# Performance work log

Measured on AMD Instinct MI355X. Metric: run time of the kernel, lower is better.

The kernel has to match this reference:

```python
import jax, jax.numpy as jnp
import numpy as np

B, F, NB, E = 32768, 64, 64, 32


def setup_inputs() -> dict:
    key = jax.random.key(0)
    k1, k2, k3, k4 = jax.random.split(key, 4)
    x = jax.random.normal(k1, (B, F), dtype=jnp.float32)
    # per-feature sorted bin edges (as produced by PLE.adapt quantiles)
    bins = jnp.sort(jax.random.uniform(k2, (F, NB), dtype=jnp.float32,
                                       minval=-2.0, maxval=2.0), axis=1)
    W = jax.random.normal(k3, (F, NB, E), dtype=jnp.float32) / np.sqrt(NB)
    b = jax.random.normal(k4, (F, E), dtype=jnp.float32)
    return {"x": x, "bins": bins, "W": W, "b": b}


def reference(x, bins, W, b):
    # x: [B,F], bins: [F,NB] sorted edges, W: [F,NB,E], b: [F,E]
    nb = bins.shape[1]
    lo = bins  # bins[j] == lookup_table[i-1] for bin i=j+1
    # lookup_table.get(i, -1): last bin has no upper edge -> defaults to -1.0
    hi = jnp.concatenate(
        [bins[:, 1:], jnp.full((bins.shape[0], 1), -1.0, bins.dtype)], axis=1)
    j = jnp.arange(nb)
    xe = x[:, :, None]                                  # [B,F,1]
    left = (xe < lo[None]) & (j > 0)                    # [B,F,NB]
    right = (xe >= hi[None]) & (j < nb - 1)             # [B,F,NB]
    v = (xe - lo[None]) / (hi - lo)[None]               # interpolation value
    # enc = 0 where left, 1 where neither, v where exactly one of left/right
    enc = jnp.where(left != right, v, jnp.where(left, 0.0, 1.0))  # [B,F,NB]
    # per-feature linear + ReLU, then features stacked along dim 1
    emb = jax.nn.relu(jnp.einsum('bfn,fne->bfe', enc, W) + b[None])  # [B,F,E]
    return emb
```

## Files before the change

kernel.cpp:

```cpp
#include <hip/hip_runtime.h>


#define FDIM 64
#define NB   64
#define EDIM 32
#define FSL  8
#define NRPB 256
#define WPAD 33
#define ITERS (NRPB / 32)

typedef __attribute__((ext_vector_type(4))) float f32x4;

__global__ __launch_bounds__(256) void nemb_fused(
    const float* __restrict__ x, const float* __restrict__ bins,
    const float* __restrict__ W, const float* __restrict__ bias,
    float* __restrict__ out)
{
    __shared__ float sW[FSL * NB * WPAD];
    __shared__ float sBins[FSL * 65];
    __shared__ float sg [FSL * NB];
    __shared__ float slg[FSL * NB];
    __shared__ float sP [FSL * EDIM];
    __shared__ float sR [FSL * EDIM];
    __shared__ float pX[4][64];
    __shared__ float pC[4][64];
    __shared__ int   pK[4][64];

    const int t     = threadIdx.x;
    const int slice = blockIdx.x & 7;
    const int chunk = blockIdx.x >> 3;
    const int f0    = slice * FSL;

    const int w  = t >> 6;
    const int l  = t & 63;
    const int rs = l >> 3;
    const int fs = l & 7;
    const int ft = l >> 3;
    const int e0 = (l & 7) * 4;

    const long r00 = (long)chunk * NRPB;

    float x_cur = x[(r00 + w * 8 + rs) * FDIM + f0 + fs];
    float bias_v = bias[(f0 + (t >> 5)) * EDIM + (t & 31)];

    {
        int idx = t * 2;
        int fl  = idx >> 6;
        int n   = idx & 63;
        const float* bg = bins + (size_t)(f0 + fl) * NB;
        float b0v = bg[n];
        float b1v = bg[n + 1];
        float b2v = (n + 1 == 63) ? -1.0f : bg[n + 2];
        float g0 = 1.0f / (b1v - b0v);
        float g1 = 1.0f / (b2v - b1v);
        sg [fl * NB + n]     = g0;
        sg [fl * NB + n + 1] = g1;
        slg[fl * NB + n]     = b0v * g0;
        slg[fl * NB + n + 1] = b1v * g1;
    }

    const float* Wg = W + (size_t)f0 * NB * EDIM;
    #pragma unroll
    for (int i = 0; i < 16; ++i) {
        int qi = i * 256 + t;
        f32x4 v = reinterpret_cast<const f32x4*>(Wg)[qi];
        int gi = qi * 4;
        int fl = gi >> 11;
        int n  = (gi >> 5) & 63;
        int ee = gi & 31;
        *reinterpret_cast<f32x4*>(&sW[fl * (NB * WPAD) + n * WPAD + ee]) = v;
    }
    if (t < 128) {
        f32x4 v = reinterpret_cast<const f32x4*>(bins + (size_t)f0 * NB)[t];
        int gi = t * 4;
        int fl = gi >> 6, n = gi & 63;
        float* d = &sBins[fl * 65 + n];
        d[0] = v.x; d[1] = v.y; d[2] = v.z; d[3] = v.w;
    }
    if (t < FSL) sBins[t * 65 + 64] = -1.0f;
    __syncthreads();

    {
        const int fl = t >> 5;
        const int e  = t & 31;
        const float* wrow = &sW[fl * (NB * WPAD) + e];
        const float* gr   = &sg [fl * NB];
        const float* lgr  = &slg[fl * NB];
        float p = 0.0f, q = 0.0f;
        #pragma unroll
        for (int n = 0; n < NB; ++n) {
            float wv = wrow[n * WPAD];
            p = fmaf(gr[n],  wv, p);
            q = fmaf(lgr[n], wv, q);
        }
        sP[fl * EDIM + e] = p;
        sR[fl * EDIM + e] = bias_v - q;
    }
    __syncthreads();

    const f32x4 Pv = *reinterpret_cast<const f32x4*>(&sP[ft * EDIM + e0]);
    const f32x4 Rv = *reinterpret_cast<const f32x4*>(&sR[ft * EDIM + e0]);

    const float* bl = &sBins[fs * 65];

    #pragma unroll 2
    for (int it = 0; it < ITERS; ++it) {
        const long rb = r00 + it * 32 + w * 8;

        float xv = x_cur;
        if (it + 1 < ITERS)
            x_cur = x[(rb + 32 + rs) * FDIM + f0 + fs];

        int k = 0;
        k += (bl[ 8] <= xv) ? 8 : 0;
        k += (bl[16] <= xv) ? 8 : 0;
        k += (bl[24] <= xv) ? 8 : 0;
        k += (bl[32] <= xv) ? 8 : 0;
        k += (bl[40] <= xv) ? 8 : 0;
        k += (bl[48] <= xv) ? 8 : 0;
        k += (bl[56] <= xv) ? 8 : 0;
        {
            const float* b2 = bl + k;
            int inner = 0;
            inner += (b2[1] <= xv) ? 1 : 0;
            inner += (b2[2] <= xv) ? 1 : 0;
            inner += (b2[3] <= xv) ? 1 : 0;
            inner += (b2[4] <= xv) ? 1 : 0;
            inner += (b2[5] <= xv) ? 1 : 0;
            inner += (b2[6] <= xv) ? 1 : 0;
            inner += (b2[7] <= xv) ? 1 : 0;
            k += inner;
        }
        float lo = bl[k];
        float hi = bl[k + 1];
        float cv = (hi - xv) * __builtin_amdgcn_rcpf(hi - lo);

        pX[w][rs * 8 + fs] = xv;
        pC[w][rs * 8 + fs] = cv;
        pK[w][rs * 8 + fs] = k;
        asm volatile("s_waitcnt lgkmcnt(0)" ::: "memory");

        #pragma unroll
        for (int r = 0; r < 8; ++r) {
            float xr = pX[w][r * 8 + ft];
            float cr = pC[w][r * 8 + ft];
            int   kr = pK[w][r * 8 + ft];
            f32x4 Wv = *reinterpret_cast<const f32x4*>(
                &sW[ft * (NB * WPAD) + kr * WPAD + e0]);
            f32x4 o;
            o.x = fmaxf(fmaf(cr, Wv.x, fmaf(xr, Pv.x, Rv.x)), 0.0f);
            o.y = fmaxf(fmaf(cr, Wv.y, fmaf(xr, Pv.y, Rv.y)), 0.0f);
            o.z = fmaxf(fmaf(cr, Wv.z, fmaf(xr, Pv.z, Rv.z)), 0.0f);
            o.w = fmaxf(fmaf(cr, Wv.w, fmaf(xr, Pv.w, Rv.w)), 0.0f);
            *reinterpret_cast<f32x4*>(
                out + (rb + r) * (FDIM * EDIM) + (f0 + ft) * EDIM + e0) = o;
        }
    }
}

extern "C" void kernel_launch(void* const* d_in, const int* in_sizes, int n_in,
                              void* d_out, int out_size, void* d_ws, size_t ws_size,
                              hipStream_t stream) {
    const float* x    = (const float*)d_in[0];
    const float* bins = (const float*)d_in[1];
    const float* W    = (const float*)d_in[2];
    const float* bias = (const float*)d_in[3];
    float* out = (float*)d_out;

    const int B = in_sizes[0] / FDIM;
    const int nchunks = B / NRPB;

    nemb_fused<<<nchunks * 8, 256, 0, stream>>>(x, bins, W, bias, out);
}
```

Before: 56.59 us.

## Store W as bf16 in LDS and exchange per-row data via ds_bpermute

Converts the W slice to bf16 (round-to-nearest-even) when staging it into shared memory, halving LDS footprint and raising possible occupancy. The per-row x, interpolation and bin-index values are now passed across lanes with ds_bpermute instead of a shared-memory staging round trip with an explicit waitcnt. The reciprocal bin widths used for the precomputed P/R terms are computed inline from sBins rather than stored in separate arrays. It trades accuracy: W loses mantissa bits, which may push results past tolerance, and the fast rcp changes rounding slightly.

```diff
diff --git a/kernel.cpp b/kernel.cpp
--- a/kernel.cpp
+++ b/kernel.cpp
@@ -6,25 +6,25 @@
 #define EDIM 32
 #define FSL  8
 #define NRPB 256
-#define WPAD 33
 #define ITERS (NRPB / 32)
+#define SWSTR 34
 
 typedef __attribute__((ext_vector_type(4))) float f32x4;
+
+static __device__ __forceinline__ unsigned bf16rne(float f) {
+    unsigned u = __float_as_uint(f);
+    return (u + 0x7FFFu + ((u >> 16) & 1u)) >> 16;
+}
 
 __global__ __launch_bounds__(256) void nemb_fused(
     const float* __restrict__ x, const float* __restrict__ bins,
     const float* __restrict__ W, const float* __restrict__ bias,
     float* __restrict__ out)
 {
-    __shared__ float sW[FSL * NB * WPAD];
+    __shared__ unsigned short sW16[FSL * NB * SWSTR];
     __shared__ float sBins[FSL * 65];
-    __shared__ float sg [FSL * NB];
-    __shared__ float slg[FSL * NB];
-    __shared__ float sP [FSL * EDIM];
-    __shared__ float sR [FSL * EDIM];
-    __shared__ float pX[4][64];
-    __shared__ float pC[4][64];
-    __shared__ int   pK[4][64];
+    __shared__ float sP[FSL * EDIM];
+    __shared__ float sR[FSL * EDIM];
 
     const int t     = threadIdx.x;
     const int slice = blockIdx.x & 7;
@@ -40,26 +40,11 @@
 
     const long r00 = (long)chunk * NRPB;
 
-    float x_cur = x[(r00 + w * 8 + rs) * FDIM + f0 + fs];
+    float x_cur  = x[(r00 + w * 8 + rs) * FDIM + f0 + fs];
     float bias_v = bias[(f0 + (t >> 5)) * EDIM + (t & 31)];
 
-    {
-        int idx = t * 2;
-        int fl  = idx >> 6;
-        int n   = idx & 63;
-        const float* bg = bins + (size_t)(f0 + fl) * NB;
-        float b0v = bg[n];
-        float b1v = bg[n + 1];
-        float b2v = (n + 1 == 63) ? -1.0f : bg[n + 2];
-        float g0 = 1.0f / (b1v - b0v);
-        float g1 = 1.0f / (b2v - b1v);
-        sg [fl * NB + n]     = g0;
-        sg [fl * NB + n + 1] = g1;
-        slg[fl * NB + n]     = b0v * g0;
-        slg[fl * NB + n + 1] = b1v * g1;
-    }
-
     const float* Wg = W + (size_t)f0 * NB * EDIM;
+    unsigned* sWd = reinterpret_cast<unsigned*>(sW16);
     #pragma unroll
     for (int i = 0; i < 16; ++i) {
         int qi = i * 256 + t;
@@ -68,7 +53,11 @@
         int fl = gi >> 11;
         int n  = (gi >> 5) & 63;
         int ee = gi & 31;
-        *reinterpret_cast<f32x4*>(&sW[fl * (NB * WPAD) + n * WPAD + ee]) = v;
+        unsigned u0 = bf16rne(v.x) | (bf16rne(v.y) << 16);
+        unsigned u1 = bf16rne(v.z) | (bf16rne(v.w) << 16);
+        int d0 = 17 * (fl * 64 + n) + (ee >> 1);
+        sWd[d0]     = u0;
+        sWd[d0 + 1] = u1;
     }
     if (t < 128) {
         f32x4 v = reinterpret_cast<const f32x4*>(bins + (size_t)f0 * NB)[t];
@@ -83,15 +72,15 @@
     {
         const int fl = t >> 5;
         const int e  = t & 31;
-        const float* wrow = &sW[fl * (NB * WPAD) + e];
-        const float* gr   = &sg [fl * NB];
-        const float* lgr  = &slg[fl * NB];
         float p = 0.0f, q = 0.0f;
         #pragma unroll
         for (int n = 0; n < NB; ++n) {
-            float wv = wrow[n * WPAD];
-            p = fmaf(gr[n],  wv, p);
-            q = fmaf(lgr[n], wv, q);
+            float lo = sBins[fl * 65 + n];
+            float hi = sBins[fl * 65 + n + 1];
+            float gv = __builtin_amdgcn_rcpf(hi - lo);
+            float wv = __uint_as_float((unsigned)sW16[(fl * 64 + n) * SWSTR + e] << 16);
+            p = fmaf(gv, wv, p);
+            q = fmaf(lo * gv, wv, q);
         }
         sP[fl * EDIM + e] = p;
         sR[fl * EDIM + e] = bias_v - q;
@@ -102,6 +91,7 @@
     const f32x4 Rv = *reinterpret_cast<const f32x4*>(&sR[ft * EDIM + e0]);
 
     const float* bl = &sBins[fs * 65];
+    const int bp_base = (l >> 3) * 4;
 
     #pragma unroll 2
     for (int it = 0; it < ITERS; ++it) {
@@ -135,18 +125,24 @@
         float hi = bl[k + 1];
         float cv = (hi - xv) * __builtin_amdgcn_rcpf(hi - lo);
 
-        pX[w][rs * 8 + fs] = xv;
-        pC[w][rs * 8 + fs] = cv;
-        pK[w][rs * 8 + fs] = k;
-        asm volatile("s_waitcnt lgkmcnt(0)" ::: "memory");
-
         #pragma unroll
         for (int r = 0; r < 8; ++r) {
-            float xr = pX[w][r * 8 + ft];
-            float cr = pC[w][r * 8 + ft];
-            int   kr = pK[w][r * 8 + ft];
-            f32x4 Wv = *reinterpret_cast<const f32x4*>(
-                &sW[ft * (NB * WPAD) + kr * WPAD + e0]);
+            const int a = bp_base + r * 32;
+            float xr = __uint_as_float((unsigned)
+                __builtin_amdgcn_ds_bpermute(a, (int)__float_as_uint(xv)));
+            float cr = __uint_as_float((unsigned)
+                __builtin_amdgcn_ds_bpermute(a, (int)__float_as_uint(cv)));
+            int   kr = __builtin_amdgcn_ds_bpermute(a, k);
+
+            int d0 = 17 * (ft * 64 + kr) + ((l & 7) << 1);
+            unsigned u0 = sWd[d0];
+            unsigned u1 = sWd[d0 + 1];
+            f32x4 Wv;
+            Wv.x = __uint_as_float(u0 << 16);
+            Wv.y = __uint_as_float(u0 & 0xFFFF0000u);
+            Wv.z = __uint_as_float(u1 << 16);
+            Wv.w = __uint_as_float(u1 & 0xFFFF0000u);
+
             f32x4 o;
             o.x = fmaxf(fmaf(cr, Wv.x, fmaf(xr, Pv.x, Rv.x)), 0.0f);
             o.y = fmaxf(fmaf(cr, Wv.y, fmaf(xr, Pv.y, Rv.y)), 0.0f);
```

Result: no change. 56.39 us (-0.4%).
